# Kernel tuning notes

Measured on AMD Instinct MI355X. Metric: run time of the kernel, lower is better.

The kernel has to match this reference:

```python
import jax, jax.numpy as jnp
import numpy as np

N, E, F, D = 50000, 800000, 128, 32
CUTOFF = 5.0


def swish(x):
    return x * jax.nn.sigmoid(x)


def setup_inputs() -> dict:
    key = jax.random.key(0)
    ks = jax.random.split(key, 15)
    sF = 1.0 / np.sqrt(F)
    inp = {
        "x": jax.random.normal(ks[0], (N, F), jnp.float32),
        # distances in [0, 6) so some edges lie beyond the 5.0 cutoff
        "rij": jax.random.uniform(ks[1], (E,), jnp.float32) * 6.0,
        "vij": jax.random.normal(ks[2], (E, 3), jnp.float32),
        "src": jax.random.randint(ks[3], (E,), 0, N),
        "dst": jax.random.randint(ks[4], (E,), 0, N),
        # transform: Dense(F,F,swish) -> Dense(F,D,swish)
        "W1": jax.random.normal(ks[5], (F, F), jnp.float32) * sF,
        "b1": jnp.zeros((F,), jnp.float32),
        "W2": jax.random.normal(ks[6], (F, D), jnp.float32) * sF,
        "b2": jnp.zeros((D,), jnp.float32),
        # transform2 (cross_product branch)
        "W1b": jax.random.normal(ks[7], (F, F), jnp.float32) * sF,
        "b1b": jnp.zeros((F,), jnp.float32),
        "W2b": jax.random.normal(ks[8], (F, D), jnp.float32) * sF,
        "b2b": jnp.zeros((D,), jnp.float32),
        # mix: Dense(3, 1), no activation
        "w_mix": jax.random.normal(ks[9], (3,), jnp.float32) * (1.0 / np.sqrt(3.0)),
        "b_mix": jnp.zeros((1,), jnp.float32),
    }
    return inp


def reference(x, rij, vij, src, dst, W1, b1, W2, b2, W1b, b1b, W2b, b2b, w_mix, b_mix):
    # node transforms: q, q2 in [N, D]
    q = swish(swish(x @ W1 + b1) @ W2 + b2)
    q2 = swish(swish(x @ W1b + b1b) @ W2b + b2b)

    # cosine cutoff on per-edge distance [E]
    c = 0.5 * (jnp.cos(jnp.pi * rij / CUTOFF) + 1.0)
    c = c * (rij < CUTOFF).astype(c.dtype)

    # e_mul_u: edge vij [E,1,3] * source-node q [E,D,1] -> [E,D,3], then cutoff scale
    mu_ij = vij[:, None, :] * q[src][:, :, None] * c[:, None, None]
    mu = jax.ops.segment_sum(mu_ij, dst, num_segments=N)  # [N,D,3]

    mu_ij2 = vij[:, None, :] * q2[src][:, :, None] * c[:, None, None]
    mu2 = jax.ops.segment_sum(mu_ij2, dst, num_segments=N)  # [N,D,3]

    mu3 = jnp.cross(mu, mu2, axis=-1)  # [N,D,3]
    stacked = jnp.stack([mu, mu2, mu3], axis=-1)  # [N,D,3,3]
    out = stacked @ w_mix + b_mix[0]  # mix Dense(3,1), squeezed -> [N,D,3]
    return out
```

## Files before the change

### kernel.cpp

```cpp
#include <hip/hip_runtime.h>
#include <hip/hip_bf16.h>

#define N_NODES 50000
#define E_EDGES 800000
#define F_DIM 128
#define D_DIM 32
#define CUTOFF 5.0f
#define PI_F 3.14159265358979f
#define SCAN_BLOCKS ((N_NODES + 255) / 256)

#define MLP_BLOCKS ((N_NODES + 31) / 32)
#define REORD_BLOCKS ((E_EDGES + 255) / 256)
#define HIST_BLOCKS ((E_EDGES / 4 + 255) / 256)
#define XS 136
#define HS 264

typedef __attribute__((ext_vector_type(8))) short bf16x8;
typedef __attribute__((ext_vector_type(4))) float f32x4;

__device__ __forceinline__ float swishf(float x) { return x / (1.0f + expf(-x)); }

__device__ __forceinline__ unsigned short f2bf(float v) {
  unsigned u = __float_as_uint(v);
  u += 0x7FFFu + ((u >> 16) & 1u);
  return (unsigned short)(u >> 16);
}
__device__ __forceinline__ float bf2f(unsigned short h) {
  return __uint_as_float(((unsigned)h) << 16);
}

__global__ __launch_bounds__(256)
void prep_hist(const float* __restrict__ W1a, const float* __restrict__ W1b,
               const float* __restrict__ W2a, const float* __restrict__ W2b,
               unsigned short* __restrict__ w1hi, unsigned short* __restrict__ w1lo,
               unsigned short* __restrict__ w2hi, unsigned short* __restrict__ w2lo,
               const float* __restrict__ rij, const int* __restrict__ dst,
               int* __restrict__ deg) {
  if (blockIdx.x < HIST_BLOCKS) {
    const int e = (blockIdx.x * 256 + threadIdx.x) * 4;
    if (e + 3 < E_EDGES) {
      const float4 r = *(const float4*)&rij[e];
      const int4 d = *(const int4*)&dst[e];
      if (r.x < CUTOFF) atomicAdd(&deg[d.x], 1);
      if (r.y < CUTOFF) atomicAdd(&deg[d.y], 1);
      if (r.z < CUTOFF) atomicAdd(&deg[d.z], 1);
      if (r.w < CUTOFF) atomicAdd(&deg[d.w], 1);
    } else if (e < E_EDGES) {
      for (int j = e; j < E_EDGES; ++j)
        if (rij[j] < CUTOFF) atomicAdd(&deg[dst[j]], 1);
    }
    return;
  }
  const int id = (blockIdx.x - HIST_BLOCKS) * 256 + threadIdx.x;
  if (id < 2 * 128 * 128) {
    const int b = id >> 14, rem = id & 16383, c = rem >> 7, k = rem & 127;
    const float v = (b ? W1b : W1a)[k * F_DIM + c];
    const unsigned short h = f2bf(v);
    w1hi[id] = h;
    w1lo[id] = f2bf(v - bf2f(h));
  }
  if (id < 2 * 32 * 128) {
    const int b = id >> 12, rem = id & 4095, c = rem >> 7, k = rem & 127;
    const float v = (b ? W2b : W2a)[k * D_DIM + c];
    const unsigned short h = f2bf(v);
    w2hi[id] = h;
    w2lo[id] = f2bf(v - bf2f(h));
  }
}

__global__ __launch_bounds__(256, 4)
void mlp_reorder(const float* __restrict__ x,
                 const unsigned short* __restrict__ w1hi, const unsigned short* __restrict__ w1lo,
                 const unsigned short* __restrict__ w2hi, const unsigned short* __restrict__ w2lo,
                 const float* __restrict__ b1a, const float* __restrict__ b1b,
                 const float* __restrict__ b2a, const float* __restrict__ b2b,
                 float* __restrict__ qq,
                 const float* __restrict__ rij, const float* __restrict__ vij,
                 const int* __restrict__ src, const int* __restrict__ dst,
                 int* __restrict__ cursor, float4* __restrict__ recs) {
  if (blockIdx.x >= MLP_BLOCKS) {
    const int e = (blockIdx.x - MLP_BLOCKS) * 256 + threadIdx.x;
    if (e >= E_EDGES) return;
    const float r = rij[e];
    if (r >= CUTOFF) return;
    const float c = 0.5f * (cosf(r * (PI_F / CUTOFF)) + 1.0f);
    const int pos = atomicAdd(&cursor[dst[e]], 1);
    recs[pos] = make_float4(c * vij[3 * e + 0], c * vij[3 * e + 1],
                            c * vij[3 * e + 2], __int_as_float(src[e]));
    return;
  }

  __shared__ unsigned short sU[2 * 32 * HS];

  const int rb = blockIdx.x * 32;
  const int t  = threadIdx.x;
  const int w  = t >> 6;
  const int l  = t & 63;
  const int lr = l & 15;
  const int kb = l >> 4;

  unsigned short* xh = sU;
  unsigned short* xl = sU + 32 * XS;

  {
    const int row = t >> 3;
    const int kq  = t & 7;
    const int rowG = min(rb + row, N_NODES - 1);
    const float* xp = x + (size_t)rowG * F_DIM;
#pragma unroll
    for (int p = 0; p < 4; ++p) {
      const int k0 = kq * 4 + p * 32;
      const float4 v = *(const float4*)&xp[k0];
      ushort4 hi4, lo4;
      hi4.x = f2bf(v.x); lo4.x = f2bf(v.x - bf2f(hi4.x));
      hi4.y = f2bf(v.y); lo4.y = f2bf(v.y - bf2f(hi4.y));
      hi4.z = f2bf(v.z); lo4.z = f2bf(v.z - bf2f(hi4.z));
      hi4.w = f2bf(v.w); lo4.w = f2bf(v.w - bf2f(hi4.w));
      *(ushort4*)&xh[row * XS + k0] = hi4;
      *(ushort4*)&xl[row * XS + k0] = lo4;
    }
  }
  __syncthreads();

  f32x4 acc[2][4];
#pragma unroll
  for (int mt = 0; mt < 2; ++mt)
#pragma unroll
    for (int ct = 0; ct < 4; ++ct) acc[mt][ct] = (f32x4){0.f, 0.f, 0.f, 0.f};

#pragma unroll
  for (int ks = 0; ks < 4; ++ks) {
    bf16x8 bh[4], bl[4];
#pragma unroll
    for (int ct = 0; ct < 4; ++ct) {
      const size_t wo = (size_t)(w * 64 + ct * 16 + lr) * 128 + ks * 32 + kb * 8;
      bh[ct] = *(const bf16x8*)&w1hi[wo];
      bl[ct] = *(const bf16x8*)&w1lo[wo];
    }
    bf16x8 ah[2], al[2];
#pragma unroll
    for (int mt = 0; mt < 2; ++mt) {
      ah[mt] = *(const bf16x8*)&xh[(mt * 16 + lr) * XS + ks * 32 + kb * 8];
      al[mt] = *(const bf16x8*)&xl[(mt * 16 + lr) * XS + ks * 32 + kb * 8];
    }
#pragma unroll
    for (int ct = 0; ct < 4; ++ct)
#pragma unroll
      for (int mt = 0; mt < 2; ++mt) {
        acc[mt][ct] = __builtin_amdgcn_mfma_f32_16x16x32_bf16(ah[mt], bh[ct], acc[mt][ct], 0, 0, 0);
        acc[mt][ct] = __builtin_amdgcn_mfma_f32_16x16x32_bf16(ah[mt], bl[ct], acc[mt][ct], 0, 0, 0);
        acc[mt][ct] = __builtin_amdgcn_mfma_f32_16x16x32_bf16(al[mt], bh[ct], acc[mt][ct], 0, 0, 0);
      }
  }

  __syncthreads();
  unsigned short* hh = sU;
  unsigned short* hl = sU + 32 * HS;

  {
    const float* b1p = (w >= 2) ? b1b : b1a;
#pragma unroll
    for (int ct = 0; ct < 4; ++ct) {
      const int colc = w * 64 + ct * 16 + lr;
      const float bias = b1p[colc & 127];
#pragma unroll
      for (int mt = 0; mt < 2; ++mt) {
#pragma unroll
        for (int rg = 0; rg < 4; ++rg) {
          const int rowr = mt * 16 + kb * 4 + rg;
          const float hv = swishf(acc[mt][ct][rg] + bias);
          const unsigned short hb = f2bf(hv);
          hh[rowr * HS + colc] = hb;
          hl[rowr * HS + colc] = f2bf(hv - bf2f(hb));
        }
      }
    }
  }
  __syncthreads();

  const int cb2 = 16 * w;
  const int br2 = cb2 >> 5;
  const int c2  = (cb2 & 31) + lr;

  f32x4 acc2[2];
  acc2[0] = (f32x4){0.f, 0.f, 0.f, 0.f};
  acc2[1] = (f32x4){0.f, 0.f, 0.f, 0.f};
#pragma unroll
  for (int ks = 0; ks < 4; ++ks) {
    const size_t w2o = (size_t)(br2 * 32 + c2) * 128 + ks * 32 + kb * 8;
    const bf16x8 bh2 = *(const bf16x8*)&w2hi[w2o];
    const bf16x8 bl2 = *(const bf16x8*)&w2lo[w2o];
    bf16x8 ah2[2], al2[2];
#pragma unroll
    for (int mt = 0; mt < 2; ++mt) {
      const int ho = (mt * 16 + lr) * HS + br2 * 128 + ks * 32 + kb * 8;
      ah2[mt] = *(const bf16x8*)&hh[ho];
      al2[mt] = *(const bf16x8*)&hl[ho];
    }
#pragma unroll
    for (int mt = 0; mt < 2; ++mt) {
      acc2[mt] = __builtin_amdgcn_mfma_f32_16x16x32_bf16(ah2[mt], bh2, acc2[mt], 0, 0, 0);
      acc2[mt] = __builtin_amdgcn_mfma_f32_16x16x32_bf16(ah2[mt], bl2, acc2[mt], 0, 0, 0);
      acc2[mt] = __builtin_amdgcn_mfma_f32_16x16x32_bf16(al2[mt], bh2, acc2[mt], 0, 0, 0);
    }
  }

  __syncthreads();
  float* sQ = (float*)sU;
  {
    const float b2v = (br2 ? b2b : b2a)[c2];
#pragma unroll
    for (int mt = 0; mt < 2; ++mt)
#pragma unroll
      for (int rg = 0; rg < 4; ++rg) {
        const int rowr = mt * 16 + kb * 4 + rg;
        sQ[rowr * 66 + 2 * c2 + br2] = swishf(acc2[mt][rg] + b2v);
      }
  }
  __syncthreads();

  {
    const int row = t >> 3;
    const int m   = t & 7;
    if (rb + row < N_NODES) {
      const float* sq = &sQ[row * 66 + m * 8];
      const float4 v0 = *(const float4*)&sq[0];
      const float4 v1 = *(const float4*)&sq[4];
      float* qp = &qq[(size_t)(rb + row) * 64 + m * 8];
      *(float4*)&qp[0] = v0;
      *(float4*)&qp[4] = v1;
    }
  }
}

__global__ __launch_bounds__(256)
void scan_blocksum(const int* __restrict__ deg, int* __restrict__ part) {
  __shared__ int red[256];
  const int t = threadIdx.x;
  const int i = blockIdx.x * 256 + t;
  red[t] = (i < N_NODES) ? deg[i] : 0;
  __syncthreads();
#pragma unroll
  for (int off = 128; off > 0; off >>= 1) {
    if (t < off) red[t] += red[t + off];
    __syncthreads();
  }
  if (t == 0) part[blockIdx.x] = red[0];
}

__global__ __launch_bounds__(256)
void scan_finish(const int* __restrict__ deg, const int* __restrict__ part,
                 int* __restrict__ row_start, int* __restrict__ cursor) {
  __shared__ int sp[256];
  __shared__ int s[256];
  const int t = threadIdx.x;
  sp[t] = (t < SCAN_BLOCKS) ? part[t] : 0;
  __syncthreads();
  for (int off = 1; off < 256; off <<= 1) {
    const int u = (t >= off) ? sp[t - off] : 0;
    __syncthreads();
    sp[t] += u;
    __syncthreads();
  }
  const int bofs = (blockIdx.x > 0) ? sp[blockIdx.x - 1] : 0;
  if (blockIdx.x == 0 && t == 0) row_start[N_NODES] = sp[SCAN_BLOCKS - 1];

  const int i = blockIdx.x * 256 + t;
  const int v = (i < N_NODES) ? deg[i] : 0;
  s[t] = v;
  __syncthreads();
  for (int off = 1; off < 256; off <<= 1) {
    const int u = (t >= off) ? s[t - off] : 0;
    __syncthreads();
    s[t] += u;
    __syncthreads();
  }
  const int excl = s[t] - v + bofs;
  if (i < N_NODES) { row_start[i] = excl; cursor[i] = excl; }
}

__global__ __launch_bounds__(256)
void gather_out(const int* __restrict__ row_start, const float4* __restrict__ recs,
                const float4* __restrict__ qq4,
                const float* __restrict__ w_mix, const float* __restrict__ b_mix,
                float* __restrict__ out) {
  const int tid = blockIdx.x * 256 + threadIdx.x;
  const int n = tid >> 4;
  const int dd = tid & 15;
  if (n >= N_NODES) return;

  const int s0 = row_start[n];
  const int s1 = row_start[n + 1];

  float a0x = 0.f, a0y = 0.f, a0z = 0.f, b0x = 0.f, b0y = 0.f, b0z = 0.f;
  float a1x = 0.f, a1y = 0.f, a1z = 0.f, b1x = 0.f, b1y = 0.f, b1z = 0.f;

  if (s1 > s0) {
    float4 rcN0 = recs[s0];
    float4 rcN1 = recs[min(s0 + 1, s1 - 1)];
    float4 rcN2 = recs[min(s0 + 2, s1 - 1)];
    float4 rcN3 = recs[min(s0 + 3, s1 - 1)];

    for (int i = s0; i < s1; i += 4) {
      const float4 rc0 = rcN0, rc1 = rcN1, rc2 = rcN2, rc3 = rcN3;
      const int j = i + 4;
      if (j < s1) {
        rcN0 = recs[j];
        rcN1 = recs[min(j + 1, s1 - 1)];
        rcN2 = recs[min(j + 2, s1 - 1)];
        rcN3 = recs[min(j + 3, s1 - 1)];
      }
      float4 q0 = qq4[(size_t)__float_as_int(rc0.w) * 16 + dd];
      float4 q1 = qq4[(size_t)__float_as_int(rc1.w) * 16 + dd];
      float4 q2 = qq4[(size_t)__float_as_int(rc2.w) * 16 + dd];
      float4 q3 = qq4[(size_t)__float_as_int(rc3.w) * 16 + dd];
      const float m1 = (i + 1 < s1) ? 1.f : 0.f;
      const float m2 = (i + 2 < s1) ? 1.f : 0.f;
      const float m3 = (i + 3 < s1) ? 1.f : 0.f;
      q1.x *= m1; q1.y *= m1; q1.z *= m1; q1.w *= m1;
      q2.x *= m2; q2.y *= m2; q2.z *= m2; q2.w *= m2;
      q3.x *= m3; q3.y *= m3; q3.z *= m3; q3.w *= m3;

      a0x += rc0.x * q0.x + rc1.x * q1.x + rc2.x * q2.x + rc3.x * q3.x;
      a0y += rc0.y * q0.x + rc1.y * q1.x + rc2.y * q2.x + rc3.y * q3.x;
      a0z += rc0.z * q0.x + rc1.z * q1.x + rc2.z * q2.x + rc3.z * q3.x;
      b0x += rc0.x * q0.y + rc1.x * q1.y + rc2.x * q2.y + rc3.x * q3.y;
      b0y += rc0.y * q0.y + rc1.y * q1.y + rc2.y * q2.y + rc3.y * q3.y;
      b0z += rc0.z * q0.y + rc1.z * q1.y + rc2.z * q2.y + rc3.z * q3.y;
      a1x += rc0.x * q0.z + rc1.x * q1.z + rc2.x * q2.z + rc3.x * q3.z;
      a1y += rc0.y * q0.z + rc1.y * q1.z + rc2.y * q2.z + rc3.y * q3.z;
      a1z += rc0.z * q0.z + rc1.z * q1.z + rc2.z * q2.z + rc3.z * q3.z;
      b1x += rc0.x * q0.w + rc1.x * q1.w + rc2.x * q2.w + rc3.x * q3.w;
      b1y += rc0.y * q0.w + rc1.y * q1.w + rc2.y * q2.w + rc3.y * q3.w;
      b1z += rc0.z * q0.w + rc1.z * q1.w + rc2.z * q2.w + rc3.z * q3.w;
    }
  }

  const float w0 = w_mix[0], w1 = w_mix[1], w2 = w_mix[2];
  const float bm = b_mix[0];

  const float c0x = a0y * b0z - a0z * b0y;
  const float c0y = a0z * b0x - a0x * b0z;
  const float c0z = a0x * b0y - a0y * b0x;
  const float c1x = a1y * b1z - a1z * b1y;
  const float c1y = a1z * b1x - a1x * b1z;
  const float c1z = a1x * b1y - a1y * b1x;

  float* op = out + (size_t)n * 96 + 6 * dd;
  op[0] = a0x * w0 + b0x * w1 + c0x * w2 + bm;
  op[1] = a0y * w0 + b0y * w1 + c0y * w2 + bm;
  op[2] = a0z * w0 + b0z * w1 + c0z * w2 + bm;
  op[3] = a1x * w0 + b1x * w1 + c1x * w2 + bm;
  op[4] = a1y * w0 + b1y * w1 + c1y * w2 + bm;
  op[5] = a1z * w0 + b1z * w1 + c1z * w2 + bm;
}

extern "C" void kernel_launch(void* const* d_in, const int* in_sizes, int n_in,
                              void* d_out, int out_size, void* d_ws, size_t ws_size,
                              hipStream_t stream) {
  const float* x     = (const float*)d_in[0];
  const float* rij   = (const float*)d_in[1];
  const float* vij   = (const float*)d_in[2];
  const int*   src   = (const int*)  d_in[3];
  const int*   dst   = (const int*)  d_in[4];
  const float* W1    = (const float*)d_in[5];
  const float* b1    = (const float*)d_in[6];
  const float* W2    = (const float*)d_in[7];
  const float* b2    = (const float*)d_in[8];
  const float* W1b   = (const float*)d_in[9];
  const float* b1b   = (const float*)d_in[10];
  const float* W2b   = (const float*)d_in[11];
  const float* b2b   = (const float*)d_in[12];
  const float* w_mix = (const float*)d_in[13];
  const float* b_mix = (const float*)d_in[14];
  float* out = (float*)d_out;

  float4* recs   = (float4*)d_ws;
  float* qq      = (float*)(recs + E_EDGES);
  int* deg       = (int*)(qq + (size_t)N_NODES * 64);
  int* cursor    = deg + N_NODES;
  int* row_start = cursor + N_NODES;
  int* part      = row_start + N_NODES + 1;

  unsigned short* w1hi = (unsigned short*)(recs + 760000);
  unsigned short* w1lo = w1hi + 2 * 128 * 128;
  unsigned short* w2hi = w1lo + 2 * 128 * 128;
  unsigned short* w2lo = w2hi + 2 * 32 * 128;

  hipMemsetAsync(deg, 0, sizeof(int) * N_NODES, stream);

  prep_hist<<<HIST_BLOCKS + SCAN_BLOCKS, 256, 0, stream>>>(
      W1, W1b, W2, W2b, w1hi, w1lo, w2hi, w2lo, rij, dst, deg);

  scan_blocksum<<<SCAN_BLOCKS, 256, 0, stream>>>(deg, part);
  scan_finish<<<SCAN_BLOCKS, 256, 0, stream>>>(deg, part, row_start, cursor);

  mlp_reorder<<<MLP_BLOCKS + REORD_BLOCKS, 256, 0, stream>>>(
      x, w1hi, w1lo, w2hi, w2lo, b1, b1b, b2, b2b, qq,
      rij, vij, src, dst, cursor, recs);

  gather_out<<<(N_NODES * 16 + 255) / 256, 256, 0, stream>>>(
      row_start, recs, (const float4*)qq, w_mix, b_mix, out);
}
```

Baseline: 234.1 us.

## Fuse memset, histogram, and two-pass scan into one cooperative kernel

```diff
diff --git a/kernel.cpp b/kernel.cpp
--- a/kernel.cpp
+++ b/kernel.cpp
@@ -1,5 +1,8 @@
 #include <hip/hip_runtime.h>
 #include <hip/hip_bf16.h>
+#include <hip/hip_cooperative_groups.h>
+
+namespace cg = cooperative_groups;
 
 #define N_NODES 50000
 #define E_EDGES 800000
@@ -11,7 +14,7 @@
 
 #define MLP_BLOCKS ((N_NODES + 31) / 32)
 #define REORD_BLOCKS ((E_EDGES + 255) / 256)
-#define HIST_BLOCKS ((E_EDGES / 4 + 255) / 256)
+#define FRONT_BLOCKS 784
 #define XS 136
 #define HS 264
 
@@ -30,14 +33,41 @@
 }
 
 __global__ __launch_bounds__(256)
-void prep_hist(const float* __restrict__ W1a, const float* __restrict__ W1b,
-               const float* __restrict__ W2a, const float* __restrict__ W2b,
-               unsigned short* __restrict__ w1hi, unsigned short* __restrict__ w1lo,
-               unsigned short* __restrict__ w2hi, unsigned short* __restrict__ w2lo,
-               const float* __restrict__ rij, const int* __restrict__ dst,
-               int* __restrict__ deg) {
-  if (blockIdx.x < HIST_BLOCKS) {
-    const int e = (blockIdx.x * 256 + threadIdx.x) * 4;
+void front(const float* __restrict__ W1a, const float* __restrict__ W1b,
+           const float* __restrict__ W2a, const float* __restrict__ W2b,
+           unsigned short* __restrict__ w1hi, unsigned short* __restrict__ w1lo,
+           unsigned short* __restrict__ w2hi, unsigned short* __restrict__ w2lo,
+           const float* __restrict__ rij, const int* __restrict__ dst,
+           int* __restrict__ deg, int* __restrict__ part,
+           int* __restrict__ row_start, int* __restrict__ cursor) {
+  cg::grid_group grid = cg::this_grid();
+  __shared__ int red[256];
+  __shared__ int sp[256];
+  __shared__ int s[256];
+
+  const int t = threadIdx.x;
+  const int gtid = blockIdx.x * 256 + t;
+  const int gsz = FRONT_BLOCKS * 256;
+
+  for (int i = gtid; i < N_NODES; i += gsz) deg[i] = 0;
+  if (gtid < 2 * 128 * 128) {
+    const int b = gtid >> 14, rem = gtid & 16383, c = rem >> 7, k = rem & 127;
+    const float v = (b ? W1b : W1a)[k * F_DIM + c];
+    const unsigned short h = f2bf(v);
+    w1hi[gtid] = h;
+    w1lo[gtid] = f2bf(v - bf2f(h));
+  }
+  if (gtid < 2 * 32 * 128) {
+    const int b = gtid >> 12, rem = gtid & 4095, c = rem >> 7, k = rem & 127;
+    const float v = (b ? W2b : W2a)[k * D_DIM + c];
+    const unsigned short h = f2bf(v);
+    w2hi[gtid] = h;
+    w2lo[gtid] = f2bf(v - bf2f(h));
+  }
+  grid.sync();
+
+  {
+    const int e = gtid * 4;
     if (e + 3 < E_EDGES) {
       const float4 r = *(const float4*)&rij[e];
       const int4 d = *(const int4*)&dst[e];
@@ -49,22 +79,46 @@
       for (int j = e; j < E_EDGES; ++j)
         if (rij[j] < CUTOFF) atomicAdd(&deg[dst[j]], 1);
     }
-    return;
-  }
-  const int id = (blockIdx.x - HIST_BLOCKS) * 256 + threadIdx.x;
-  if (id < 2 * 128 * 128) {
-    const int b = id >> 14, rem = id & 16383, c = rem >> 7, k = rem & 127;
-    const float v = (b ? W1b : W1a)[k * F_DIM + c];
-    const unsigned short h = f2bf(v);
-    w1hi[id] = h;
-    w1lo[id] = f2bf(v - bf2f(h));
-  }
-  if (id < 2 * 32 * 128) {
-    const int b = id >> 12, rem = id & 4095, c = rem >> 7, k = rem & 127;
-    const float v = (b ? W2b : W2a)[k * D_DIM + c];
-    const unsigned short h = f2bf(v);
-    w2hi[id] = h;
-    w2lo[id] = f2bf(v - bf2f(h));
+  }
+  grid.sync();
+
+  if (blockIdx.x < SCAN_BLOCKS) {
+    const int i = blockIdx.x * 256 + t;
+    red[t] = (i < N_NODES) ? deg[i] : 0;
+    __syncthreads();
+#pragma unroll
+    for (int off = 128; off > 0; off >>= 1) {
+      if (t < off) red[t] += red[t + off];
+      __syncthreads();
+    }
+    if (t == 0) part[blockIdx.x] = red[0];
+  }
+  grid.sync();
+
+  if (blockIdx.x < SCAN_BLOCKS) {
+    sp[t] = (t < SCAN_BLOCKS) ? part[t] : 0;
+    __syncthreads();
+    for (int off = 1; off < 256; off <<= 1) {
+      const int u = (t >= off) ? sp[t - off] : 0;
+      __syncthreads();
+      sp[t] += u;
+      __syncthreads();
+    }
+    const int bofs = (blockIdx.x > 0) ? sp[blockIdx.x - 1] : 0;
+    if (blockIdx.x == 0 && t == 0) row_start[N_NODES] = sp[SCAN_BLOCKS - 1];
+
+    const int i = blockIdx.x * 256 + t;
+    const int v = (i < N_NODES) ? deg[i] : 0;
+    s[t] = v;
+    __syncthreads();
+    for (int off = 1; off < 256; off <<= 1) {
+      const int u = (t >= off) ? s[t - off] : 0;
+      __syncthreads();
+      s[t] += u;
+      __syncthreads();
+    }
+    const int excl = s[t] - v + bofs;
+    if (i < N_NODES) { row_start[i] = excl; cursor[i] = excl; }
   }
 }
 
@@ -234,52 +288,6 @@
 }
 
 __global__ __launch_bounds__(256)
-void scan_blocksum(const int* __restrict__ deg, int* __restrict__ part) {
-  __shared__ int red[256];
-  const int t = threadIdx.x;
-  const int i = blockIdx.x * 256 + t;
-  red[t] = (i < N_NODES) ? deg[i] : 0;
-  __syncthreads();
-#pragma unroll
-  for (int off = 128; off > 0; off >>= 1) {
-    if (t < off) red[t] += red[t + off];
-    __syncthreads();
-  }
-  if (t == 0) part[blockIdx.x] = red[0];
-}
-
-__global__ __launch_bounds__(256)
-void scan_finish(const int* __restrict__ deg, const int* __restrict__ part,
-                 int* __restrict__ row_start, int* __restrict__ cursor) {
-  __shared__ int sp[256];
-  __shared__ int s[256];
-  const int t = threadIdx.x;
-  sp[t] = (t < SCAN_BLOCKS) ? part[t] : 0;
-  __syncthreads();
-  for (int off = 1; off < 256; off <<= 1) {
-    const int u = (t >= off) ? sp[t - off] : 0;
-    __syncthreads();
-    sp[t] += u;
-    __syncthreads();
-  }
-  const int bofs = (blockIdx.x > 0) ? sp[blockIdx.x - 1] : 0;
-  if (blockIdx.x == 0 && t == 0) row_start[N_NODES] = sp[SCAN_BLOCKS - 1];
-
-  const int i = blockIdx.x * 256 + t;
-  const int v = (i < N_NODES) ? deg[i] : 0;
-  s[t] = v;
-  __syncthreads();
-  for (int off = 1; off < 256; off <<= 1) {
-    const int u = (t >= off) ? s[t - off] : 0;
-    __syncthreads();
-    s[t] += u;
-    __syncthreads();
-  }
-  const int excl = s[t] - v + bofs;
-  if (i < N_NODES) { row_start[i] = excl; cursor[i] = excl; }
-}
-
-__global__ __launch_bounds__(256)
 void gather_out(const int* __restrict__ row_start, const float4* __restrict__ recs,
                 const float4* __restrict__ qq4,
                 const float* __restrict__ w_mix, const float* __restrict__ b_mix,
@@ -387,13 +395,16 @@
   unsigned short* w2hi = w1lo + 2 * 128 * 128;
   unsigned short* w2lo = w2hi + 2 * 32 * 128;
 
-  hipMemsetAsync(deg, 0, sizeof(int) * N_NODES, stream);
-
-  prep_hist<<<HIST_BLOCKS + SCAN_BLOCKS, 256, 0, stream>>>(
-      W1, W1b, W2, W2b, w1hi, w1lo, w2hi, w2lo, rij, dst, deg);
-
-  scan_blocksum<<<SCAN_BLOCKS, 256, 0, stream>>>(deg, part);
-  scan_finish<<<SCAN_BLOCKS, 256, 0, stream>>>(deg, part, row_start, cursor);
+  {
+    void* args[] = {
+      (void*)&W1, (void*)&W1b, (void*)&W2, (void*)&W2b,
+      (void*)&w1hi, (void*)&w1lo, (void*)&w2hi, (void*)&w2lo,
+      (void*)&rij, (void*)&dst,
+      (void*)&deg, (void*)&part, (void*)&row_start, (void*)&cursor
+    };
+    hipLaunchCooperativeKernel((const void*)front, dim3(FRONT_BLOCKS), dim3(256),
+                               args, 0, stream);
+  }
 
   mlp_reorder<<<MLP_BLOCKS + REORD_BLOCKS, 256, 0, stream>>>(
       x, w1hi, w1lo, w2hi, w2lo, b1, b1b, b2, b2b, qq,
```

After: 479.5 us. 105% more time.

## Fuse degree scan into histogram kernel via last-block ticket and shrink MLP tile

Applied to the files above, without the earlier changes.

```diff
diff --git a/kernel.cpp b/kernel.cpp
--- a/kernel.cpp
+++ b/kernel.cpp
@@ -7,11 +7,13 @@
 #define D_DIM 32
 #define CUTOFF 5.0f
 #define PI_F 3.14159265358979f
-#define SCAN_BLOCKS ((N_NODES + 255) / 256)
-
-#define MLP_BLOCKS ((N_NODES + 31) / 32)
+
+#define MLP_ROWS 16
+#define MLP_BLOCKS (N_NODES / MLP_ROWS)
 #define REORD_BLOCKS ((E_EDGES + 255) / 256)
 #define HIST_BLOCKS ((E_EDGES / 4 + 255) / 256)
+#define PREP_BLOCKS 128
+#define SCAN_CH 196
 #define XS 136
 #define HS 264
 
@@ -30,14 +32,37 @@
 }
 
 __global__ __launch_bounds__(256)
-void prep_hist(const float* __restrict__ W1a, const float* __restrict__ W1b,
-               const float* __restrict__ W2a, const float* __restrict__ W2b,
-               unsigned short* __restrict__ w1hi, unsigned short* __restrict__ w1lo,
-               unsigned short* __restrict__ w2hi, unsigned short* __restrict__ w2lo,
-               const float* __restrict__ rij, const int* __restrict__ dst,
-               int* __restrict__ deg) {
-  if (blockIdx.x < HIST_BLOCKS) {
-    const int e = (blockIdx.x * 256 + threadIdx.x) * 4;
+void prep_hist_scan(const float* __restrict__ W1a, const float* __restrict__ W1b,
+                    const float* __restrict__ W2a, const float* __restrict__ W2b,
+                    unsigned short* __restrict__ w1hi, unsigned short* __restrict__ w1lo,
+                    unsigned short* __restrict__ w2hi, unsigned short* __restrict__ w2lo,
+                    const float* __restrict__ rij, const int* __restrict__ dst,
+                    int* __restrict__ deg, int* __restrict__ done,
+                    int* __restrict__ cursor, int* __restrict__ row_start,
+                    int* __restrict__ scratch) {
+  const int t = threadIdx.x;
+
+  if (blockIdx.x >= HIST_BLOCKS) {
+    const int id = (blockIdx.x - HIST_BLOCKS) * 256 + t;
+    if (id < 2 * 128 * 128) {
+      const int b = id >> 14, rem = id & 16383, c = rem >> 7, k = rem & 127;
+      const float v = (b ? W1b : W1a)[k * F_DIM + c];
+      const unsigned short h = f2bf(v);
+      w1hi[id] = h;
+      w1lo[id] = f2bf(v - bf2f(h));
+    }
+    if (id < 2 * 32 * 128) {
+      const int b = id >> 12, rem = id & 4095, c = rem >> 7, k = rem & 127;
+      const float v = (b ? W2b : W2a)[k * D_DIM + c];
+      const unsigned short h = f2bf(v);
+      w2hi[id] = h;
+      w2lo[id] = f2bf(v - bf2f(h));
+    }
+    return;
+  }
+
+  {
+    const int e = (blockIdx.x * 256 + t) * 4;
     if (e + 3 < E_EDGES) {
       const float4 r = *(const float4*)&rij[e];
       const int4 d = *(const int4*)&dst[e];
@@ -49,26 +74,47 @@
       for (int j = e; j < E_EDGES; ++j)
         if (rij[j] < CUTOFF) atomicAdd(&deg[dst[j]], 1);
     }
-    return;
-  }
-  const int id = (blockIdx.x - HIST_BLOCKS) * 256 + threadIdx.x;
-  if (id < 2 * 128 * 128) {
-    const int b = id >> 14, rem = id & 16383, c = rem >> 7, k = rem & 127;
-    const float v = (b ? W1b : W1a)[k * F_DIM + c];
-    const unsigned short h = f2bf(v);
-    w1hi[id] = h;
-    w1lo[id] = f2bf(v - bf2f(h));
-  }
-  if (id < 2 * 32 * 128) {
-    const int b = id >> 12, rem = id & 4095, c = rem >> 7, k = rem & 127;
-    const float v = (b ? W2b : W2a)[k * D_DIM + c];
-    const unsigned short h = f2bf(v);
-    w2hi[id] = h;
-    w2lo[id] = f2bf(v - bf2f(h));
-  }
-}
-
-__global__ __launch_bounds__(256, 4)
+  }
+
+  __threadfence();
+  __syncthreads();
+  __shared__ int ticket;
+  if (t == 0) ticket = atomicAdd(done, 1);
+  __syncthreads();
+  if (ticket != HIST_BLOCKS - 1) return;
+
+  __shared__ int sc[256];
+  const int base = t * SCAN_CH;
+  int sum = 0;
+  for (int i = 0; i < SCAN_CH; ++i) {
+    const int idx = base + i;
+    if (idx < N_NODES) {
+      const int v = atomicAdd(&deg[idx], 0);
+      scratch[idx] = v;
+      sum += v;
+    }
+  }
+  sc[t] = sum;
+  __syncthreads();
+  for (int off = 1; off < 256; off <<= 1) {
+    const int u = (t >= off) ? sc[t - off] : 0;
+    __syncthreads();
+    sc[t] += u;
+    __syncthreads();
+  }
+  int run = sc[t] - sum;
+  if (t == 255) row_start[N_NODES] = sc[255];
+  for (int i = 0; i < SCAN_CH; ++i) {
+    const int idx = base + i;
+    if (idx < N_NODES) {
+      row_start[idx] = run;
+      cursor[idx] = run;
+      run += scratch[idx];
+    }
+  }
+}
+
+__global__ __launch_bounds__(256, 8)
 void mlp_reorder(const float* __restrict__ x,
                  const unsigned short* __restrict__ w1hi, const unsigned short* __restrict__ w1lo,
                  const unsigned short* __restrict__ w2hi, const unsigned short* __restrict__ w2lo,
@@ -90,9 +136,9 @@
     return;
   }
 
-  __shared__ unsigned short sU[2 * 32 * HS];
-
-  const int rb = blockIdx.x * 32;
+  __shared__ unsigned short sU[2 * MLP_ROWS * HS];
+
+  const int rb = blockIdx.x * MLP_ROWS;
   const int t  = threadIdx.x;
   const int w  = t >> 6;
   const int l  = t & 63;
@@ -100,16 +146,15 @@
   const int kb = l >> 4;
 
   unsigned short* xh = sU;
-  unsigned short* xl = sU + 32 * XS;
-
-  {
-    const int row = t >> 3;
-    const int kq  = t & 7;
-    const int rowG = min(rb + row, N_NODES - 1);
-    const float* xp = x + (size_t)rowG * F_DIM;
-#pragma unroll
-    for (int p = 0; p < 4; ++p) {
-      const int k0 = kq * 4 + p * 32;
+  unsigned short* xl = sU + MLP_ROWS * XS;
+
+  {
+    const int row = t >> 4;
+    const int kq  = t & 15;
+    const float* xp = x + (size_t)(rb + row) * F_DIM;
+#pragma unroll
+    for (int p = 0; p < 2; ++p) {
+      const int k0 = kq * 4 + p * 64;
       const float4 v = *(const float4*)&xp[k0];
       ushort4 hi4, lo4;
       hi4.x = f2bf(v.x); lo4.x = f2bf(v.x - bf2f(hi4.x));
@@ -122,40 +167,28 @@
   }
   __syncthreads();
 
-  f32x4 acc[2][4];
-#pragma unroll
-  for (int mt = 0; mt < 2; ++mt)
-#pragma unroll
-    for (int ct = 0; ct < 4; ++ct) acc[mt][ct] = (f32x4){0.f, 0.f, 0.f, 0.f};
+  f32x4 acc[4];
+#pragma unroll
+  for (int ct = 0; ct < 4; ++ct) acc[ct] = (f32x4){0.f, 0.f, 0.f, 0.f};
 
 #pragma unroll
   for (int ks = 0; ks < 4; ++ks) {
-    bf16x8 bh[4], bl[4];
+    const bf16x8 ah = *(const bf16x8*)&xh[lr * XS + ks * 32 + kb * 8];
+    const bf16x8 al = *(const bf16x8*)&xl[lr * XS + ks * 32 + kb * 8];
 #pragma unroll
     for (int ct = 0; ct < 4; ++ct) {
       const size_t wo = (size_t)(w * 64 + ct * 16 + lr) * 128 + ks * 32 + kb * 8;
-      bh[ct] = *(const bf16x8*)&w1hi[wo];
-      bl[ct] = *(const bf16x8*)&w1lo[wo];
-    }
-    bf16x8 ah[2], al[2];
-#pragma unroll
-    for (int mt = 0; mt < 2; ++mt) {
-      ah[mt] = *(const bf16x8*)&xh[(mt * 16 + lr) * XS + ks * 32 + kb * 8];
-      al[mt] = *(const bf16x8*)&xl[(mt * 16 + lr) * XS + ks * 32 + kb * 8];
-    }
-#pragma unroll
-    for (int ct = 0; ct < 4; ++ct)
-#pragma unroll
-      for (int mt = 0; mt < 2; ++mt) {
-        acc[mt][ct] = __builtin_amdgcn_mfma_f32_16x16x32_bf16(ah[mt], bh[ct], acc[mt][ct], 0, 0, 0);
-        acc[mt][ct] = __builtin_amdgcn_mfma_f32_16x16x32_bf16(ah[mt], bl[ct], acc[mt][ct], 0, 0, 0);
-        acc[mt][ct] = __builtin_amdgcn_mfma_f32_16x16x32_bf16(al[mt], bh[ct], acc[mt][ct], 0, 0, 0);
-      }
+      const bf16x8 bh = *(const bf16x8*)&w1hi[wo];
+      const bf16x8 bl = *(const bf16x8*)&w1lo[wo];
+      acc[ct] = __builtin_amdgcn_mfma_f32_16x16x32_bf16(ah, bh, acc[ct], 0, 0, 0);
+      acc[ct] = __builtin_amdgcn_mfma_f32_16x16x32_bf16(ah, bl, acc[ct], 0, 0, 0);
+      acc[ct] = __builtin_amdgcn_mfma_f32_16x16x32_bf16(al, bh, acc[ct], 0, 0, 0);
+    }
   }
 
   __syncthreads();
   unsigned short* hh = sU;
-  unsigned short* hl = sU + 32 * HS;
+  unsigned short* hl = sU + MLP_ROWS * HS;
 
   {
     const float* b1p = (w >= 2) ? b1b : b1a;
@@ -164,45 +197,32 @@
       const int colc = w * 64 + ct * 16 + lr;
       const float bias = b1p[colc & 127];
 #pragma unroll
-      for (int mt = 0; mt < 2; ++mt) {
-#pragma unroll
-        for (int rg = 0; rg < 4; ++rg) {
-          const int rowr = mt * 16 + kb * 4 + rg;
-          const float hv = swishf(acc[mt][ct][rg] + bias);
-          const unsigned short hb = f2bf(hv);
-          hh[rowr * HS + colc] = hb;
-          hl[rowr * HS + colc] = f2bf(hv - bf2f(hb));
-        }
+      for (int rg = 0; rg < 4; ++rg) {
+        const int rowr = kb * 4 + rg;
+        const float hv = swishf(acc[ct][rg] + bias);
+        const unsigned short hb = f2bf(hv);
+        hh[rowr * HS + colc] = hb;
+        hl[rowr * HS + colc] = f2bf(hv - bf2f(hb));
       }
     }
   }
   __syncthreads();
 
-  const int cb2 = 16 * w;
-  const int br2 = cb2 >> 5;
-  const int c2  = (cb2 & 31) + lr;
-
-  f32x4 acc2[2];
-  acc2[0] = (f32x4){0.f, 0.f, 0.f, 0.f};
-  acc2[1] = (f32x4){0.f, 0.f, 0.f, 0.f};
+  const int br2 = w >> 1;
+  const int c2  = (w & 1) * 16 + lr;
+
+  f32x4 acc2 = (f32x4){0.f, 0.f, 0.f, 0.f};
 #pragma unroll
   for (int ks = 0; ks < 4; ++ks) {
     const size_t w2o = (size_t)(br2 * 32 + c2) * 128 + ks * 32 + kb * 8;
     const bf16x8 bh2 = *(const bf16x8*)&w2hi[w2o];
     const bf16x8 bl2 = *(const bf16x8*)&w2lo[w2o];
-    bf16x8 ah2[2], al2[2];
-#pragma unroll
-    for (int mt = 0; mt < 2; ++mt) {
-      const int ho = (mt * 16 + lr) * HS + br2 * 128 + ks * 32 + kb * 8;
-      ah2[mt] = *(const bf16x8*)&hh[ho];
-      al2[mt] = *(const bf16x8*)&hl[ho];
-    }
-#pragma unroll
-    for (int mt = 0; mt < 2; ++mt) {
-      acc2[mt] = __builtin_amdgcn_mfma_f32_16x16x32_bf16(ah2[mt], bh2, acc2[mt], 0, 0, 0);
-      acc2[mt] = __builtin_amdgcn_mfma_f32_16x16x32_bf16(ah2[mt], bl2, acc2[mt], 0, 0, 0);
-      acc2[mt] = __builtin_amdgcn_mfma_f32_16x16x32_bf16(al2[mt], bh2, acc2[mt], 0, 0, 0);
-    }
+    const int ho = lr * HS + br2 * 128 + ks * 32 + kb * 8;
+    const bf16x8 ah2 = *(const bf16x8*)&hh[ho];
+    const bf16x8 al2 = *(const bf16x8*)&hl[ho];
+    acc2 = __builtin_amdgcn_mfma_f32_16x16x32_bf16(ah2, bh2, acc2, 0, 0, 0);
+    acc2 = __builtin_amdgcn_mfma_f32_16x16x32_bf16(ah2, bl2, acc2, 0, 0, 0);
+    acc2 = __builtin_amdgcn_mfma_f32_16x16x32_bf16(al2, bh2, acc2, 0, 0, 0);
   }
 
   __syncthreads();
@@ -210,73 +230,19 @@
   {
     const float b2v = (br2 ? b2b : b2a)[c2];
 #pragma unroll
-    for (int mt = 0; mt < 2; ++mt)
-#pragma unroll
-      for (int rg = 0; rg < 4; ++rg) {
-        const int rowr = mt * 16 + kb * 4 + rg;
-        sQ[rowr * 66 + 2 * c2 + br2] = swishf(acc2[mt][rg] + b2v);
-      }
-  }
-  __syncthreads();
-
-  {
-    const int row = t >> 3;
-    const int m   = t & 7;
-    if (rb + row < N_NODES) {
-      const float* sq = &sQ[row * 66 + m * 8];
-      const float4 v0 = *(const float4*)&sq[0];
-      const float4 v1 = *(const float4*)&sq[4];
-      float* qp = &qq[(size_t)(rb + row) * 64 + m * 8];
-      *(float4*)&qp[0] = v0;
-      *(float4*)&qp[4] = v1;
-    }
-  }
-}
-
-__global__ __launch_bounds__(256)
-void scan_blocksum(const int* __restrict__ deg, int* __restrict__ part) {
-  __shared__ int red[256];
-  const int t = threadIdx.x;
-  const int i = blockIdx.x * 256 + t;
-  red[t] = (i < N_NODES) ? deg[i] : 0;
-  __syncthreads();
-#pragma unroll
-  for (int off = 128; off > 0; off >>= 1) {
-    if (t < off) red[t] += red[t + off];
-    __syncthreads();
-  }
-  if (t == 0) part[blockIdx.x] = red[0];
-}
-
-__global__ __launch_bounds__(256)
-void scan_finish(const int* __restrict__ deg, const int* __restrict__ part,
-                 int* __restrict__ row_start, int* __restrict__ cursor) {
-  __shared__ int sp[256];
-  __shared__ int s[256];
-  const int t = threadIdx.x;
-  sp[t] = (t < SCAN_BLOCKS) ? part[t] : 0;
-  __syncthreads();
-  for (int off = 1; off < 256; off <<= 1) {
-    const int u = (t >= off) ? sp[t - off] : 0;
-    __syncthreads();
-    sp[t] += u;
-    __syncthreads();
-  }
-  const int bofs = (blockIdx.x > 0) ? sp[blockIdx.x - 1] : 0;
-  if (blockIdx.x == 0 && t == 0) row_start[N_NODES] = sp[SCAN_BLOCKS - 1];
-
-  const int i = blockIdx.x * 256 + t;
-  const int v = (i < N_NODES) ? deg[i] : 0;
-  s[t] = v;
-  __syncthreads();
-  for (int off = 1; off < 256; off <<= 1) {
-    const int u = (t >= off) ? s[t - off] : 0;
-    __syncthreads();
-    s[t] += u;
-    __syncthreads();
-  }
-  const int excl = s[t] - v + bofs;
-  if (i < N_NODES) { row_start[i] = excl; cursor[i] = excl; }
+    for (int rg = 0; rg < 4; ++rg) {
+      const int rowr = kb * 4 + rg;
+      sQ[rowr * 66 + 2 * c2 + br2] = swishf(acc2[rg] + b2v);
+    }
+  }
+  __syncthreads();
+
+  {
+    const int row = t >> 4;
+    const int m   = t & 15;
+    *(float4*)&qq[(size_t)(rb + row) * 64 + m * 4] =
+        *(const float4*)&sQ[row * 66 + m * 4];
+  }
 }
 
 __global__ __launch_bounds__(256)
@@ -378,22 +344,21 @@
   float4* recs   = (float4*)d_ws;
   float* qq      = (float*)(recs + E_EDGES);
   int* deg       = (int*)(qq + (size_t)N_NODES * 64);
-  int* cursor    = deg + N_NODES;
+  int* done      = deg + N_NODES;
+  int* cursor    = done + 1;
   int* row_start = cursor + N_NODES;
-  int* part      = row_start + N_NODES + 1;
+  int* scratch   = row_start + N_NODES + 1;
 
   unsigned short* w1hi = (unsigned short*)(recs + 760000);
   unsigned short* w1lo = w1hi + 2 * 128 * 128;
   unsigned short* w2hi = w1lo + 2 * 128 * 128;
   unsigned short* w2lo = w2hi + 2 * 32 * 128;
 
-  hipMemsetAsync(deg, 0, sizeof(int) * N_NODES, stream);
-
-  prep_hist<<<HIST_BLOCKS + SCAN_BLOCKS, 256, 0, stream>>>(
-      W1, W1b, W2, W2b, w1hi, w1lo, w2hi, w2lo, rij, dst, deg);
-
-  scan_blocksum<<<SCAN_BLOCKS, 256, 0, stream>>>(deg, part);
-  scan_finish<<<SCAN_BLOCKS, 256, 0, stream>>>(deg, part, row_start, cursor);
+  hipMemsetAsync(deg, 0, sizeof(int) * (N_NODES + 1), stream);
+
+  prep_hist_scan<<<HIST_BLOCKS + PREP_BLOCKS, 256, 0, stream>>>(
+      W1, W1b, W2, W2b, w1hi, w1lo, w2hi, w2lo,
+      rij, dst, deg, done, cursor, row_start, scratch);
 
   mlp_reorder<<<MLP_BLOCKS + REORD_BLOCKS, 256, 0, stream>>>(
       x, w1hi, w1lo, w2hi, w2lo, b1, b1b, b2, b2b, qq,
```

Result: slower. 474.9 us (+102.9%).
